# Kernel tuning notes

Measured on AMD Instinct MI355X. Metric: run time of the kernel, lower is better.

## Reference

```python
import jax, jax.numpy as jnp
import numpy as np

WINDOW_SIZE = 11
SIGMA = 1.5

def _gauss1d(n, sigma):
    xs = (jnp.arange(n) - n // 2).astype(jnp.float32)
    g = jnp.exp(-(xs ** 2) / (2.0 * sigma ** 2))
    return g / g.sum()

def _blur3d(v, g):
    # Separable 3D Gaussian blur == dense outer-product 3D window used by the
    # original (the torch window is an exact outer product of 1D gaussians).
    C = v.shape[1]
    k = g.shape[0]
    p = k // 2
    for ax in range(3):
        kshape = [1, 1, 1]
        kshape[ax] = k
        w = jnp.broadcast_to(g.reshape(tuple(kshape))[None, None], (C, 1) + tuple(kshape))
        pad = [(0, 0), (0, 0), (0, 0)]
        pad[ax] = (p, p)
        v = jax.lax.conv_general_dilated(
            v, w, window_strides=(1, 1, 1), padding=pad,
            dimension_numbers=('NCDHW', 'OIDHW', 'NCDHW'),
            feature_group_count=C)
    return v

def _ssim(a, b, size_average=True):
    g = _gauss1d(WINDOW_SIZE, SIGMA)
    mu1 = _blur3d(a, g)
    mu2 = _blur3d(b, g)
    mu1_sq = mu1 * mu1
    mu2_sq = mu2 * mu2
    sigma1_sq = _blur3d(a * a, g) - mu1_sq
    sigma2_sq = _blur3d(b * b, g) - mu2_sq
    sigma12 = _blur3d(a * b, g) - mu1 * mu2
    C1, C2 = 0.01 ** 2, 0.03 ** 2
    ssim_map = ((2.0 * mu1 * mu2 + C1) * (2.0 * sigma12 + C2)) / \
               ((mu1_sq + mu2_sq + C1) * (sigma1_sq + sigma2_sq + C2))
    if size_average:
        return ssim_map.mean()
    return ssim_map.mean(axis=(1, 2, 3))

def reference(x, y, z, modality):
    # modality: 0 -> 'PET' (compare x vs z), 1 -> 'CT' (compare x vs y)
    if modality == 0:
        s = _ssim(x, z)
    else:
        s = _ssim(x, y)
    return (1.0 - s) ** 2

def setup_inputs() -> dict:
    key = jax.random.key(0)
    k1, k2, k3 = jax.random.split(key, 3)
    shape = (2, 1, 192, 192, 192)
    x = jax.random.uniform(k1, shape, dtype=jnp.float32)
    y = jax.random.uniform(k2, shape, dtype=jnp.float32)
    z = jax.random.uniform(k3, shape, dtype=jnp.float32)
    return {"x": x, "y": y, "z": z, "modality": 0}
```

## Files before the change

kernel.cpp:

```cpp
#include <hip/hip_runtime.h>
#include <math.h>

#define NW 192
#define NH 192
#define ND 192
#define NB 2
#define SLICE (NH * NW)
#define SLICEB (SLICE * 4)
#define VOLB (ND * SLICEB)
#define VOLF ((double)(NB) * ND * NH * NW)
#define NF4 (NW / 4)

#define TH 16
#define TW 16
#define HALO 5
#define LHH (TH + 2 * HALO)
#define DC 24
#define NITER ((DC + 2 * HALO) / 2)
#define TPS (LHH * (TW / 4))
#define NTASK (2 * TPS)
#define WTILES (NW / TW)
#define HTILES (NH / TH)
#define DCHUNKS (ND / DC)
#define TILES (WTILES * HTILES)
#define NBLOCKS (TILES * DCHUNKS * NB)
#define NXCD 8
#define CPX (NBLOCKS / NXCD)

#define FPAD 424
#define TWSZ (10 * FPAD)
#define HB_PSTR 264
#define HBSZ (10 * HB_PSTR)

typedef float f32x4 __attribute__((ext_vector_type(4)));
typedef int   i32x4 __attribute__((ext_vector_type(4)));

__device__ f32x4 llvm_buf_load_x4(i32x4 rsrc, int voffset, int soffset, int aux)
    __asm("llvm.amdgcn.raw.buffer.load.v4f32");

__device__ __forceinline__ i32x4 make_srd(const void* p, unsigned bytes) {
    union { i32x4 v; struct { const void* p; unsigned nrec; unsigned fl; } s; } u;
    u.s.p = p;
    u.s.nrec = bytes;
    u.s.fl = 0x00020000;
    return u.v;
}

__device__ unsigned g_done = 0;

struct GaussK { float g[11]; };

template <bool FAST>
__device__ __forceinline__ float ssim_tile(
    const float* __restrict__ xb, const float* __restrict__ bb,
    int h0, int w0, int d0, const GaussK& G, float* tw, float* hbuf, int tid)
{
    const int tx = tid & 15, ty = tid >> 4;
    const bool is_strip = (tid < NTASK);
    const int s_of = tid / TPS;
    const int r_of = (tid % TPS) >> 2;
    const int c_of = tid & 3;
    const int gh = h0 - HALO + r_of;
    const int f4base = (w0 >> 2) + c_of - 2;
    float* twp = tw + s_of * 5 * FPAD + r_of * TW + 4 * c_of;

    const bool is_col = (tid < 160);
    const float* cbase = tw + (tid >> 4) * FPAD + (tid & 15);
    float* hwr = hbuf + (tid >> 4) * HB_PSTR + (tid & 15);
    const float* hrd = hbuf + ty * TW + tx;

    const i32x4 rsA = make_srd(xb, VOLB);
    const i32x4 rsB = make_srd(bb, VOLB);
    const int wb = gh * (NW * 4) + f4base * 16;
    const int offbase = (d0 - HALO + s_of) * SLICEB + wb;
    const bool row_ok = is_strip && ((unsigned)gh < (unsigned)NH);
    const long rowb4 = (long)gh * NF4;
    const f32x4* xb4 = (const f32x4*)xb;
    const f32x4* bb4 = (const f32x4*)bb;

    float acc0[12], acc1[12], acc2[12], acc3[12], acc4[12];
#pragma unroll
    for (int j = 0; j < 12; ++j) { acc0[j]=0.f; acc1[j]=0.f; acc2[j]=0.f; acc3[j]=0.f; acc4[j]=0.f; }
    float sum = 0.f;

    auto d_round = [&](const float* vA, const float* vB, int J) {
#pragma unroll
        for (int j = 0; j < 11; ++j) {
            const float g = G.g[j];
            acc0[j] += g * vA[0]; acc1[j] += g * vA[1]; acc2[j] += g * vA[2];
            acc3[j] += g * vA[3]; acc4[j] += g * vA[4];
        }
#pragma unroll
        for (int j = 1; j < 12; ++j) {
            const float g = G.g[j - 1];
            acc0[j] += g * vB[0]; acc1[j] += g * vB[1]; acc2[j] += g * vB[2];
            acc3[j] += g * vB[3]; acc4[j] += g * vB[4];
        }
        if (J >= 5) {
#pragma unroll
            for (int e = 0; e < 2; ++e) {
                const float mu1 = acc0[e], mu2 = acc1[e];
                const float mu1sq = mu1 * mu1, mu2sq = mu2 * mu2, mu12 = mu1 * mu2;
                const float s1 = acc2[e] - mu1sq;
                const float s2 = acc3[e] - mu2sq;
                const float s12 = acc4[e] - mu12;
                const float C1 = 1e-4f, C2 = 9e-4f;
                const float num = (2.f * mu12 + C1) * (2.f * s12 + C2);
                const float den = (mu1sq + mu2sq + C1) * (s1 + s2 + C2);
                sum += num * __builtin_amdgcn_rcpf(den);
            }
        }
#pragma unroll
        for (int j = 0; j < 10; ++j) {
            acc0[j] = acc0[j+2]; acc1[j] = acc1[j+2]; acc2[j] = acc2[j+2];
            acc3[j] = acc3[j+2]; acc4[j] = acc4[j+2];
        }
        acc0[10]=0.f; acc1[10]=0.f; acc2[10]=0.f; acc3[10]=0.f; acc4[10]=0.f;
        acc0[11]=0.f; acc1[11]=0.f; acc2[11]=0.f; acc3[11]=0.f; acc4[11]=0.f;
    };

#pragma unroll 1
    for (int it = 0; it < NITER; ++it) {
        f32x4 pa[5], pb[5];
        if (is_strip) {
            if (FAST) {
                const int off = offbase + it * (2 * SLICEB);
#pragma unroll
                for (int k = 0; k < 5; ++k) {
                    pa[k] = llvm_buf_load_x4(rsA, off + 16 * k, 0, 0);
                    pb[k] = llvm_buf_load_x4(rsB, off + 16 * k, 0, 0);
                }
            } else {
                const int dd = d0 - HALO + 2 * it + s_of;
                const bool okd = row_ok && ((unsigned)dd < (unsigned)ND);
                const long sb4 = (long)dd * (SLICE / 4) + rowb4;
#pragma unroll
                for (int k = 0; k < 5; ++k) {
                    const int f4 = f4base + k;
                    const bool ok = okd && ((unsigned)f4 < (unsigned)NF4);
                    f32x4 va = {0.f, 0.f, 0.f, 0.f}, vb = {0.f, 0.f, 0.f, 0.f};
                    if (ok) { va = xb4[sb4 + f4]; vb = bb4[sb4 + f4]; }
                    pa[k] = va; pb[k] = vb;
                }
            }
        }

        if (it > 0) {
            float vA[5], vB[5];
#pragma unroll
            for (int f = 0; f < 5; ++f) {
                vA[f] = hrd[f * HB_PSTR];
                vB[f] = hrd[(5 + f) * HB_PSTR];
            }
            d_round(vA, vB, it - 1);
        }

        if (is_strip) {
            float A[4]={0,0,0,0}, Bv[4]={0,0,0,0}, A2[4]={0,0,0,0},
                  B2[4]={0,0,0,0}, AB[4]={0,0,0,0};
#pragma unroll
            for (int k = 0; k < 5; ++k) {
#pragma unroll
                for (int e = 0; e < 4; ++e) {
                    const int idx = 4 * k + e;
                    if (idx < 3 || idx > 16) continue;
                    const float a = pa[k][e];
                    const float b = pb[k][e];
                    const float a2 = a * a, b2 = b * b, ab = a * b;
#pragma unroll
                    for (int j = 0; j < 4; ++j) {
                        const int u = idx - 3 - j;
                        if (u < 0 || u > 10) continue;
                        const float g = G.g[u];
                        A[j]  += g * a;  Bv[j] += g * b;
                        A2[j] += g * a2; B2[j] += g * b2; AB[j] += g * ab;
                    }
                }
            }
            ((float4*)(twp + 0 * FPAD))[0] = make_float4(A[0], A[1], A[2], A[3]);
            ((float4*)(twp + 1 * FPAD))[0] = make_float4(Bv[0], Bv[1], Bv[2], Bv[3]);
            ((float4*)(twp + 2 * FPAD))[0] = make_float4(A2[0], A2[1], A2[2], A2[3]);
            ((float4*)(twp + 3 * FPAD))[0] = make_float4(B2[0], B2[1], B2[2], B2[3]);
            ((float4*)(twp + 4 * FPAD))[0] = make_float4(AB[0], AB[1], AB[2], AB[3]);
        }
        __syncthreads();

        if (is_col) {
            float o[16];
#pragma unroll
            for (int r = 0; r < 16; ++r) o[r] = 0.f;
#pragma unroll
            for (int r = 0; r < 26; ++r) {
                const float w = cbase[r * TW];
                const int jlo = (r - 10 < 0) ? 0 : r - 10;
                const int jhi = (r < 15) ? r : 15;
#pragma unroll
                for (int j = jlo; j <= jhi; ++j) o[j] += G.g[r - j] * w;
            }
#pragma unroll
            for (int r = 0; r < 16; ++r) hwr[r * TW] = o[r];
        }
        __syncthreads();
    }

    {
        float vA[5], vB[5];
#pragma unroll
        for (int f = 0; f < 5; ++f) {
            vA[f] = hrd[f * HB_PSTR];
            vB[f] = hrd[(5 + f) * HB_PSTR];
        }
        d_round(vA, vB, NITER - 1);
    }
    return sum;
}

__global__ __launch_bounds__(256)
void k_ssim_fused(const float* __restrict__ x, const float* __restrict__ y,
                  const float* __restrict__ z, const int* __restrict__ mod,
                  float* __restrict__ out, GaussK G)
{
    __shared__ float tw[TWSZ];
    __shared__ float hbuf[HBSZ];
    __shared__ float wred[4];

    const int tid = threadIdx.x;

    const unsigned lin = blockIdx.x +
        (unsigned)gridDim.x * (blockIdx.y + (unsigned)gridDim.y * blockIdx.z);
    const unsigned work = (lin & (NXCD - 1)) * CPX + (lin >> 3);
    const unsigned tile = work % TILES;
    const unsigned rest = work / TILES;
    const int wt = tile % WTILES, ht = tile / WTILES;
    const int d0 = (int)(rest % DCHUNKS) * DC;
    const int n  = (int)(rest / DCHUNKS);
    const int h0 = ht * TH, w0 = wt * TW;

    const float* bsel = (*mod == 0) ? z : y;
    const float* xb = x + (size_t)n * ND * SLICE;
    const float* bb = bsel + (size_t)n * ND * SLICE;

    const bool interior = (ht > 0) & (ht < HTILES - 1) & (wt > 0) & (wt < WTILES - 1);
    float sum;
    if (interior) sum = ssim_tile<true >(xb, bb, h0, w0, d0, G, tw, hbuf, tid);
    else          sum = ssim_tile<false>(xb, bb, h0, w0, d0, G, tw, hbuf, tid);

    float v = sum;
#pragma unroll
    for (int off = 32; off > 0; off >>= 1) v += __shfl_down(v, off, 64);
    if ((tid & 63) == 0) wred[tid >> 6] = v;
    __syncthreads();
    if (tid == 0) {
        const float bsum = wred[0] + wred[1] + wred[2] + wred[3];
        atomicAdd(out, bsum);
        __threadfence();
        unsigned old = atomicAdd(&g_done, 1u);
        if (old == (unsigned)(NBLOCKS - 1)) {
            float total = atomicAdd(out, 0.f);
            double m = 1.0 - (double)total / VOLF;
            out[0] = (float)(m * m);
            __threadfence();
            atomicExch(&g_done, 0u);
        }
    }
}

extern "C" void kernel_launch(void* const* d_in, const int* in_sizes, int n_in,
                              void* d_out, int out_size, void* d_ws, size_t ws_size,
                              hipStream_t stream) {
    const float* x = (const float*)d_in[0];
    const float* y = (const float*)d_in[1];
    const float* z = (const float*)d_in[2];
    const int* modality = (const int*)d_in[3];
    float* out = (float*)d_out;

    GaussK G;
    {
        double raw[11], s = 0.0;
        for (int i = 0; i < 11; ++i) {
            double dx = (double)(i - 5);
            raw[i] = exp(-(dx * dx) / (2.0 * 1.5 * 1.5));
            s += raw[i];
        }
        for (int i = 0; i < 11; ++i) G.g[i] = (float)(raw[i] / s);
    }

    dim3 grid(TILES, DCHUNKS, NB);
    k_ssim_fused<<<grid, 256, 0, stream>>>(x, y, z, modality, out, G);
}
```

Before: 349.4 us.

## Double-buffer LDS stages, drop one barrier per iteration, swizzle banks, deepen depth chunk

Double-buffers the W-pass and H-pass shared-memory tiles so that only one __syncthreads is needed per depth iteration. The depth accumulation now lags the H-pass by one iteration, with register prefetch of the values it needs. LDS strides change from padding to an XOR parity swizzle meant to avoid bank conflicts. The depth chunk doubles from 24 to 48, which cuts the redundant halo reloads but halves the block count and doubles LDS use.

```diff
diff --git a/kernel.cpp b/kernel.cpp
--- a/kernel.cpp
+++ b/kernel.cpp
@@ -15,7 +15,7 @@
 #define TW 16
 #define HALO 5
 #define LHH (TH + 2 * HALO)
-#define DC 24
+#define DC 48
 #define NITER ((DC + 2 * HALO) / 2)
 #define TPS (LHH * (TW / 4))
 #define NTASK (2 * TPS)
@@ -27,10 +27,10 @@
 #define NXCD 8
 #define CPX (NBLOCKS / NXCD)
 
-#define FPAD 424
-#define TWSZ (10 * FPAD)
-#define HB_PSTR 264
-#define HBSZ (10 * HB_PSTR)
+#define FSTR 416
+#define TWBUF (10 * FSTR)
+#define HB_PSTR 256
+#define HBBUF (10 * HB_PSTR)
 
 typedef float f32x4 __attribute__((ext_vector_type(4)));
 typedef int   i32x4 __attribute__((ext_vector_type(4)));
@@ -53,7 +53,7 @@
 template <bool FAST>
 __device__ __forceinline__ float ssim_tile(
     const float* __restrict__ xb, const float* __restrict__ bb,
-    int h0, int w0, int d0, const GaussK& G, float* tw, float* hbuf, int tid)
+    int h0, int w0, int d0, const GaussK& G, float* tw, float* hb, int tid)
 {
     const int tx = tid & 15, ty = tid >> 4;
     const bool is_strip = (tid < NTASK);
@@ -62,12 +62,19 @@
     const int c_of = tid & 3;
     const int gh = h0 - HALO + r_of;
     const int f4base = (w0 >> 2) + c_of - 2;
-    float* twp = tw + s_of * 5 * FPAD + r_of * TW + 4 * c_of;
+
+    const int tw_wo_e = s_of * 5 * FSTR + ((r_of ^ (s_of & 1)) << 4) + 4 * c_of;
+    const int tw_wo_o = tw_wo_e ^ 16;
 
     const bool is_col = (tid < 160);
-    const float* cbase = tw + (tid >> 4) * FPAD + (tid & 15);
-    float* hwr = hbuf + (tid >> 4) * HB_PSTR + (tid & 15);
-    const float* hrd = hbuf + ty * TW + tx;
+    const int cp = tid >> 4, cc = tid & 15;
+    const int cpar = (cp & 1) << 4;
+    const int cr_e = cp * FSTR + cc + cpar;
+    const int cr_o = cp * FSTR + cc - cpar;
+    const int hw_e = cp * HB_PSTR + cc + cpar;
+    const int hw_o = cp * HB_PSTR + cc - cpar;
+    const int gr_e = (ty << 4) + tx;
+    const int gr_o = ((ty << 4) ^ 16) + tx;
 
     const i32x4 rsA = make_srd(xb, VOLB);
     const i32x4 rsB = make_srd(bb, VOLB);
@@ -81,20 +88,22 @@
     float acc0[12], acc1[12], acc2[12], acc3[12], acc4[12];
 #pragma unroll
     for (int j = 0; j < 12; ++j) { acc0[j]=0.f; acc1[j]=0.f; acc2[j]=0.f; acc3[j]=0.f; acc4[j]=0.f; }
+    float vGA[5] = {0.f,0.f,0.f,0.f,0.f};
+    float vGB[5] = {0.f,0.f,0.f,0.f,0.f};
     float sum = 0.f;
 
-    auto d_round = [&](const float* vA, const float* vB, int J) {
+    auto d_round = [&](int J) {
 #pragma unroll
         for (int j = 0; j < 11; ++j) {
             const float g = G.g[j];
-            acc0[j] += g * vA[0]; acc1[j] += g * vA[1]; acc2[j] += g * vA[2];
-            acc3[j] += g * vA[3]; acc4[j] += g * vA[4];
+            acc0[j] += g * vGA[0]; acc1[j] += g * vGA[1]; acc2[j] += g * vGA[2];
+            acc3[j] += g * vGA[3]; acc4[j] += g * vGA[4];
         }
 #pragma unroll
         for (int j = 1; j < 12; ++j) {
             const float g = G.g[j - 1];
-            acc0[j] += g * vB[0]; acc1[j] += g * vB[1]; acc2[j] += g * vB[2];
-            acc3[j] += g * vB[3]; acc4[j] += g * vB[4];
+            acc0[j] += g * vGB[0]; acc1[j] += g * vGB[1]; acc2[j] += g * vGB[2];
+            acc3[j] += g * vGB[3]; acc4[j] += g * vGB[4];
         }
         if (J >= 5) {
 #pragma unroll
@@ -121,6 +130,10 @@
 
 #pragma unroll 1
     for (int it = 0; it < NITER; ++it) {
+        float* twb = tw + (it & 1) * TWBUF;
+        float* hwb = hb + (it & 1) * HBBUF;
+        const float* hrb = hb + ((it + 1) & 1) * HBBUF;
+
         f32x4 pa[5], pb[5];
         if (is_strip) {
             if (FAST) {
@@ -145,15 +158,7 @@
             }
         }
 
-        if (it > 0) {
-            float vA[5], vB[5];
-#pragma unroll
-            for (int f = 0; f < 5; ++f) {
-                vA[f] = hrd[f * HB_PSTR];
-                vB[f] = hrd[(5 + f) * HB_PSTR];
-            }
-            d_round(vA, vB, it - 1);
-        }
+        if (it >= 2) d_round(it - 2);
 
         if (is_strip) {
             float A[4]={0,0,0,0}, Bv[4]={0,0,0,0}, A2[4]={0,0,0,0},
@@ -177,11 +182,11 @@
                     }
                 }
             }
-            ((float4*)(twp + 0 * FPAD))[0] = make_float4(A[0], A[1], A[2], A[3]);
-            ((float4*)(twp + 1 * FPAD))[0] = make_float4(Bv[0], Bv[1], Bv[2], Bv[3]);
-            ((float4*)(twp + 2 * FPAD))[0] = make_float4(A2[0], A2[1], A2[2], A2[3]);
-            ((float4*)(twp + 3 * FPAD))[0] = make_float4(B2[0], B2[1], B2[2], B2[3]);
-            ((float4*)(twp + 4 * FPAD))[0] = make_float4(AB[0], AB[1], AB[2], AB[3]);
+            ((float4*)(twb + tw_wo_e + 0 * FSTR))[0] = make_float4(A[0], A[1], A[2], A[3]);
+            ((float4*)(twb + tw_wo_o + 1 * FSTR))[0] = make_float4(Bv[0], Bv[1], Bv[2], Bv[3]);
+            ((float4*)(twb + tw_wo_e + 2 * FSTR))[0] = make_float4(A2[0], A2[1], A2[2], A2[3]);
+            ((float4*)(twb + tw_wo_o + 3 * FSTR))[0] = make_float4(B2[0], B2[1], B2[2], B2[3]);
+            ((float4*)(twb + tw_wo_e + 4 * FSTR))[0] = make_float4(AB[0], AB[1], AB[2], AB[3]);
         }
         __syncthreads();
 
@@ -191,27 +196,37 @@
             for (int r = 0; r < 16; ++r) o[r] = 0.f;
 #pragma unroll
             for (int r = 0; r < 26; ++r) {
-                const float w = cbase[r * TW];
+                const float w = twb[(r & 1 ? cr_o : cr_e) + (r << 4)];
                 const int jlo = (r - 10 < 0) ? 0 : r - 10;
                 const int jhi = (r < 15) ? r : 15;
 #pragma unroll
                 for (int j = jlo; j <= jhi; ++j) o[j] += G.g[r - j] * w;
             }
 #pragma unroll
-            for (int r = 0; r < 16; ++r) hwr[r * TW] = o[r];
-        }
-        __syncthreads();
+            for (int r = 0; r < 16; ++r)
+                hwb[(r & 1 ? hw_o : hw_e) + (r << 4)] = o[r];
+        }
+
+        if (it >= 1) {
+#pragma unroll
+            for (int f = 0; f < 5; ++f) {
+                vGA[f] = hrb[(f & 1 ? gr_o : gr_e) + f * HB_PSTR];
+                vGB[f] = hrb[((f & 1) ? gr_e : gr_o) + (5 + f) * HB_PSTR];
+            }
+        }
     }
 
+    d_round(NITER - 2);
+    __syncthreads();
     {
-        float vA[5], vB[5];
+        const float* hrb = hb + ((NITER - 1) & 1) * HBBUF;
 #pragma unroll
         for (int f = 0; f < 5; ++f) {
-            vA[f] = hrd[f * HB_PSTR];
-            vB[f] = hrd[(5 + f) * HB_PSTR];
-        }
-        d_round(vA, vB, NITER - 1);
+            vGA[f] = hrb[(f & 1 ? gr_o : gr_e) + f * HB_PSTR];
+            vGB[f] = hrb[((f & 1) ? gr_e : gr_o) + (5 + f) * HB_PSTR];
+        }
     }
+    d_round(NITER - 1);
     return sum;
 }
 
@@ -220,8 +235,8 @@
                   const float* __restrict__ z, const int* __restrict__ mod,
                   float* __restrict__ out, GaussK G)
 {
-    __shared__ float tw[TWSZ];
-    __shared__ float hbuf[HBSZ];
+    __shared__ float tw[2 * TWBUF];
+    __shared__ float hb[2 * HBBUF];
     __shared__ float wred[4];
 
     const int tid = threadIdx.x;
@@ -242,8 +257,8 @@
 
     const bool interior = (ht > 0) & (ht < HTILES - 1) & (wt > 0) & (wt < WTILES - 1);
     float sum;
-    if (interior) sum = ssim_tile<true >(xb, bb, h0, w0, d0, G, tw, hbuf, tid);
-    else          sum = ssim_tile<false>(xb, bb, h0, w0, d0, G, tw, hbuf, tid);
+    if (interior) sum = ssim_tile<true >(xb, bb, h0, w0, d0, G, tw, hb, tid);
+    else          sum = ssim_tile<false>(xb, bb, h0, w0, d0, G, tw, hb, tid);
 
     float v = sum;
 #pragma unroll
```

Result: slower. 359.3 us (+2.8%).

## Double depth chunk and replace LDS padding with XOR row swizzle

Applied to the files above, without the earlier changes.

The depth chunk per block grows from 24 to 48 slices, so the 10-slice depth halo is amortised over more output slices and less redundant loading and blurring is done. This also halves the number of blocks. The padded LDS strides are replaced with unpadded strides plus an XOR swizzle on row parity to avoid bank conflicts. The cost is fewer blocks for occupancy and load balance, longer per-block loops, and extra index arithmetic.

```diff
diff --git a/kernel.cpp b/kernel.cpp
--- a/kernel.cpp
+++ b/kernel.cpp
@@ -15,7 +15,7 @@
 #define TW 16
 #define HALO 5
 #define LHH (TH + 2 * HALO)
-#define DC 24
+#define DC 48
 #define NITER ((DC + 2 * HALO) / 2)
 #define TPS (LHH * (TW / 4))
 #define NTASK (2 * TPS)
@@ -27,9 +27,9 @@
 #define NXCD 8
 #define CPX (NBLOCKS / NXCD)
 
-#define FPAD 424
-#define TWSZ (10 * FPAD)
-#define HB_PSTR 264
+#define FSTR 416
+#define TWSZ (10 * FSTR)
+#define HB_PSTR 256
 #define HBSZ (10 * HB_PSTR)
 
 typedef float f32x4 __attribute__((ext_vector_type(4)));
@@ -62,12 +62,19 @@
     const int c_of = tid & 3;
     const int gh = h0 - HALO + r_of;
     const int f4base = (w0 >> 2) + c_of - 2;
-    float* twp = tw + s_of * 5 * FPAD + r_of * TW + 4 * c_of;
+
+    const int tw_wo_e = s_of * 5 * FSTR + ((r_of ^ (s_of & 1)) << 4) + 4 * c_of;
+    const int tw_wo_o = tw_wo_e ^ 16;
 
     const bool is_col = (tid < 160);
-    const float* cbase = tw + (tid >> 4) * FPAD + (tid & 15);
-    float* hwr = hbuf + (tid >> 4) * HB_PSTR + (tid & 15);
-    const float* hrd = hbuf + ty * TW + tx;
+    const int cp = tid >> 4, cc = tid & 15;
+    const int cpar = (cp & 1) << 4;
+    const int cr_e = cp * FSTR + cc + cpar;
+    const int cr_o = cp * FSTR + cc - cpar;
+    const int hw_e = cp * HB_PSTR + cc + cpar;
+    const int hw_o = cp * HB_PSTR + cc - cpar;
+    const int gr_e = (ty << 4) + tx;
+    const int gr_o = ((ty << 4) ^ 16) + tx;
 
     const i32x4 rsA = make_srd(xb, VOLB);
     const i32x4 rsB = make_srd(bb, VOLB);
@@ -149,8 +156,8 @@
             float vA[5], vB[5];
 #pragma unroll
             for (int f = 0; f < 5; ++f) {
-                vA[f] = hrd[f * HB_PSTR];
-                vB[f] = hrd[(5 + f) * HB_PSTR];
+                vA[f] = hbuf[(f & 1 ? gr_o : gr_e) + f * HB_PSTR];
+                vB[f] = hbuf[((f & 1) ? gr_e : gr_o) + (5 + f) * HB_PSTR];
             }
             d_round(vA, vB, it - 1);
         }
@@ -177,11 +184,11 @@
                     }
                 }
             }
-            ((float4*)(twp + 0 * FPAD))[0] = make_float4(A[0], A[1], A[2], A[3]);
-            ((float4*)(twp + 1 * FPAD))[0] = make_float4(Bv[0], Bv[1], Bv[2], Bv[3]);
-            ((float4*)(twp + 2 * FPAD))[0] = make_float4(A2[0], A2[1], A2[2], A2[3]);
-            ((float4*)(twp + 3 * FPAD))[0] = make_float4(B2[0], B2[1], B2[2], B2[3]);
-            ((float4*)(twp + 4 * FPAD))[0] = make_float4(AB[0], AB[1], AB[2], AB[3]);
+            ((float4*)(tw + tw_wo_e + 0 * FSTR))[0] = make_float4(A[0], A[1], A[2], A[3]);
+            ((float4*)(tw + tw_wo_o + 1 * FSTR))[0] = make_float4(Bv[0], Bv[1], Bv[2], Bv[3]);
+            ((float4*)(tw + tw_wo_e + 2 * FSTR))[0] = make_float4(A2[0], A2[1], A2[2], A2[3]);
+            ((float4*)(tw + tw_wo_o + 3 * FSTR))[0] = make_float4(B2[0], B2[1], B2[2], B2[3]);
+            ((float4*)(tw + tw_wo_e + 4 * FSTR))[0] = make_float4(AB[0], AB[1], AB[2], AB[3]);
         }
         __syncthreads();
 
@@ -191,14 +198,15 @@
             for (int r = 0; r < 16; ++r) o[r] = 0.f;
 #pragma unroll
             for (int r = 0; r < 26; ++r) {
-                const float w = cbase[r * TW];
+                const float w = tw[(r & 1 ? cr_o : cr_e) + (r << 4)];
                 const int jlo = (r - 10 < 0) ? 0 : r - 10;
                 const int jhi = (r < 15) ? r : 15;
 #pragma unroll
                 for (int j = jlo; j <= jhi; ++j) o[j] += G.g[r - j] * w;
             }
 #pragma unroll
-            for (int r = 0; r < 16; ++r) hwr[r * TW] = o[r];
+            for (int r = 0; r < 16; ++r)
+                hbuf[(r & 1 ? hw_o : hw_e) + (r << 4)] = o[r];
         }
         __syncthreads();
     }
@@ -207,8 +215,8 @@
         float vA[5], vB[5];
 #pragma unroll
         for (int f = 0; f < 5; ++f) {
-            vA[f] = hrd[f * HB_PSTR];
-            vB[f] = hrd[(5 + f) * HB_PSTR];
+            vA[f] = hbuf[(f & 1 ? gr_o : gr_e) + f * HB_PSTR];
+            vB[f] = hbuf[((f & 1) ? gr_e : gr_o) + (5 + f) * HB_PSTR];
         }
         d_round(vA, vB, NITER - 1);
     }
```

New measurement: 353.4 us. No clear change (+1.2%).
